# Kernel tuning notes

Hardware: AMD Instinct MI355X
Metric: run time of the kernel (lower is better)

Reference implementation:

```python
import jax, jax.numpy as jnp
import numpy as np

B, S, D = 4, 2048, 1024
H, E = 16, 64  # n_heads, head_size; H*E == D


def setup_inputs() -> dict:
    key = jax.random.key(0)
    ks = jax.random.split(key, 6)
    sd = 1.0 / np.sqrt(D)
    x = jax.random.normal(ks[0], (B, S, D), dtype=jnp.float32)
    # per-head Q/K/V projection weights, stacked: [H, D, E]
    Wq = jax.random.uniform(ks[1], (H, D, E), jnp.float32, -sd, sd)
    Wk = jax.random.uniform(ks[2], (H, D, E), jnp.float32, -sd, sd)
    Wv = jax.random.uniform(ks[3], (H, D, E), jnp.float32, -sd, sd)
    Wp = jax.random.uniform(ks[4], (D, D), jnp.float32, -sd, sd)
    bp = jax.random.uniform(ks[5], (D,), jnp.float32, -sd, sd)
    return {"x": x, "Wq": Wq, "Wk": Wk, "Wv": Wv, "Wp": Wp, "bp": bp}


def reference(x, Wq, Wk, Wv, Wp, bp):
    # Per-head projections (all heads batched): [B, H, S, E]
    q = jnp.einsum('bsd,hde->bhse', x, Wq)
    k = jnp.einsum('bsd,hde->bhse', x, Wk)
    v = jnp.einsum('bsd,hde->bhse', x, Wv)
    scale = E ** -0.5
    # Full causal score matrix [B, H, S, S]
    wei = jnp.einsum('bhse,bhte->bhst', q, k) * scale
    causal = jnp.tril(jnp.ones((S, S), dtype=bool))
    wei = jnp.where(causal, wei, -jnp.inf)
    wei = jax.nn.softmax(wei, axis=-1)
    out = jnp.einsum('bhst,bhte->bhse', wei, v)
    # concat heads along feature dim: [B, S, H*E]
    out = out.transpose(0, 2, 1, 3).reshape(B, S, H * E)
    # output projection (dropout is identity in eval)
    return out @ Wp.T + bp
```

## Files before the change

kernel.cpp:

```cpp
#include <hip/hip_runtime.h>

#define B_ 4
#define S_ 2048
#define D_ 1024
#define H_ 16
#define E_ 64
#define M_ (B_*S_)

typedef __attribute__((ext_vector_type(8))) short short8;
typedef __attribute__((ext_vector_type(4))) float floatx4;

#define GLD16(g, l) __builtin_amdgcn_global_load_lds( \
    (const __attribute__((address_space(1))) unsigned*)(g), \
    (__attribute__((address_space(3))) unsigned*)(l), 16, 0, 0)

__device__ __forceinline__ ushort f2b(float f) {
    union { float f; unsigned u; } v; v.f = f;
    unsigned r = v.u + 0x7fffu + ((v.u >> 16) & 1u);
    return (ushort)(r >> 16);
}
__device__ __forceinline__ unsigned cvt_pk_bf16(float lo, float hi) {
    unsigned r;
    asm("v_cvt_pk_bf16_f32 %0, %1, %2" : "=v"(r) : "v"(lo), "v"(hi));
    return r;
}
__device__ __forceinline__ float fast_exp2(float x) {
#if __has_builtin(__builtin_amdgcn_exp2f)
    return __builtin_amdgcn_exp2f(x);
#else
    float r; asm("v_exp_f32 %0, %1" : "=v"(r) : "v"(x)); return r;
#endif
}
__device__ __forceinline__ float lane_pull(float v, int srclane) {
    return __int_as_float(__builtin_amdgcn_ds_bpermute(srclane << 2, __float_as_int(v)));
}

__global__ __launch_bounds__(256) void cast_bf16(const float* __restrict__ in,
                                                 ushort* __restrict__ out, int n8) {
    int i = blockIdx.x * 256 + threadIdx.x;
    int stride = gridDim.x * 256;
    for (; i < n8; i += stride) {
        float4 a = ((const float4*)in)[2 * i];
        float4 b = ((const float4*)in)[2 * i + 1];
        short8 o;
        o[0] = (short)f2b(a.x); o[1] = (short)f2b(a.y);
        o[2] = (short)f2b(a.z); o[3] = (short)f2b(a.w);
        o[4] = (short)f2b(b.x); o[5] = (short)f2b(b.y);
        o[6] = (short)f2b(b.z); o[7] = (short)f2b(b.w);
        ((short8*)out)[i] = o;
    }
}

__global__ __launch_bounds__(256) void transpose_w(const float* __restrict__ Wq,
                                                   const float* __restrict__ Wk,
                                                   const float* __restrict__ Wv,
                                                   ushort* __restrict__ wt) {
    int g = blockIdx.y;
    int d0 = blockIdx.x * 64;
    const float* W = (g < 16 ? Wq : (g < 32 ? Wk : Wv)) + (size_t)(g & 15) * (D_ * E_);
    __shared__ __align__(16) ushort T[64 * 80];
    int t = threadIdx.x;
    #pragma unroll
    for (int it = 0; it < 4; ++it) {
        int i = it * 256 + t;
        int r = i >> 4, c = i & 15;
        float4 x = *(const float4*)(W + (size_t)(d0 + r) * E_ + c * 4);
        T[(c * 4 + 0) * 80 + r] = f2b(x.x);
        T[(c * 4 + 1) * 80 + r] = f2b(x.y);
        T[(c * 4 + 2) * 80 + r] = f2b(x.z);
        T[(c * 4 + 3) * 80 + r] = f2b(x.w);
    }
    __syncthreads();
    #pragma unroll
    for (int it = 0; it < 2; ++it) {
        int i = it * 256 + t;
        int e = i >> 3, c = i & 7;
        short8 x = *(const short8*)&T[e * 80 + c * 8];
        *(short8*)&wt[((size_t)g * E_ + e) * D_ + d0 + c * 8] = x;
    }
}

__global__ __launch_bounds__(512) void gemm_qkv(const ushort* __restrict__ xb,
                                                const ushort* __restrict__ wt,
                                                ushort* __restrict__ qk,
                                                ushort* __restrict__ vt) {
    const int m0 = blockIdx.x * 256;
    const int n0 = blockIdx.y * 128;
    const int w  = n0 >> 10;

    __shared__ __align__(16) ushort As[256 * 32];
    __shared__ __align__(16) ushort Bs[128 * 32];

    const int t = threadIdx.x, l = t & 63, wid = t >> 6;
    const int wm = (wid & 3) * 64, wn = (wid >> 2) * 64;
    floatx4 acc[4][4] = {};

    for (int k0 = 0; k0 < D_; k0 += 32) {
        __syncthreads();
        #pragma unroll
        for (int it = 0; it < 2; ++it) {
            int i = it * 512 + t;
            int r = i >> 2, cs = i & 3;
            int c = cs ^ ((r >> 1) & 3);
            GLD16(xb + (size_t)(m0 + r) * D_ + k0 + c * 8, &As[i * 8]);
        }
        {
            int r = t >> 2, cs = t & 3;
            int c = cs ^ ((r >> 1) & 3);
            GLD16(wt + (size_t)(n0 + r) * D_ + k0 + c * 8, &Bs[t * 8]);
        }
        __syncthreads();

        short8 af[4], bf[4];
        #pragma unroll
        for (int mf = 0; mf < 4; ++mf) {
            int row = wm + 16 * mf + (l & 15);
            int c = (l >> 4) ^ ((row >> 1) & 3);
            af[mf] = *(const short8*)&As[row * 32 + c * 8];
        }
        #pragma unroll
        for (int nf = 0; nf < 4; ++nf) {
            int row = wn + 16 * nf + (l & 15);
            int c = (l >> 4) ^ ((row >> 1) & 3);
            bf[nf] = *(const short8*)&Bs[row * 32 + c * 8];
        }
        #pragma unroll
        for (int mf = 0; mf < 4; ++mf)
            #pragma unroll
            for (int nf = 0; nf < 4; ++nf)
                acc[mf][nf] = __builtin_amdgcn_mfma_f32_16x16x32_bf16(af[mf], bf[nf], acc[mf][nf], 0, 0, 0);
    }

    if (w < 2) {
        ushort* outw = qk + (size_t)w * ((size_t)B_ * H_ * S_ * E_);
        #pragma unroll
        for (int mf = 0; mf < 4; ++mf)
            #pragma unroll
            for (int nf = 0; nf < 4; ++nf) {
                int n = n0 + wn + 16 * nf + (l & 15);
                int h = (n >> 6) & 15, e = n & 63;
                #pragma unroll
                for (int r = 0; r < 4; ++r) {
                    int m = m0 + wm + 16 * mf + (l >> 4) * 4 + r;
                    int b = m >> 11, s = m & (S_ - 1);
                    outw[((size_t)((b << 4) + h) * S_ + s) * E_ + e] = f2b(acc[mf][nf][r]);
                }
            }
    } else {
        #pragma unroll
        for (int mf = 0; mf < 4; ++mf) {
            int m = m0 + wm + 16 * mf + (l >> 4) * 4;
            int b = m >> 11, s = m & (S_ - 1);
            #pragma unroll
            for (int nf = 0; nf < 4; ++nf) {
                int n = n0 + wn + 16 * nf + (l & 15);
                int h = (n >> 6) & 15, e = n & 63;
                unsigned pk0 = cvt_pk_bf16(acc[mf][nf][0], acc[mf][nf][1]);
                unsigned pk1 = cvt_pk_bf16(acc[mf][nf][2], acc[mf][nf][3]);
                *(uint2*)&vt[((size_t)((b << 4) + h) * E_ + e) * S_ + s] = make_uint2(pk0, pk1);
            }
        }
    }
}

__global__ __launch_bounds__(256) void flash(const ushort* __restrict__ qg,
                                             const ushort* __restrict__ kg,
                                             const ushort* __restrict__ vtg,
                                             ushort* __restrict__ attn) {
    const int n = blockIdx.x;
    const int x = n >> 6;
    const int bh = n & 63;
    const int b = bh >> 4, h = bh & 15;
    const ushort* qb = qg + (size_t)bh * (S_ * E_);
    const ushort* kb = kg + (size_t)bh * (S_ * E_);
    const ushort* vb = vtg + (size_t)bh * (E_ * S_);

    __shared__ __align__(16) ushort QP[64 * 64];
    __shared__ __align__(16) ushort Ks[2][64 * 64];
    __shared__ __align__(16) ushort Vs[2][64 * 64];

    const int t = threadIdx.x, l = t & 63, wid = t >> 6;
    const float SC = 0.18033688f;
    const float NEG_INF = -__builtin_inff();
    const int g = l >> 4;
    const int qloc = l & 15;
    const int qts[2] = {x, 31 - x};
    ushort* Pw = &QP[wid * 1024];

    #pragma unroll 1
    for (int qi = 0; qi < 2; ++qi) {
        const int qt = qts[qi];

        #pragma unroll
        for (int it = 0; it < 2; ++it) {
            int i = it * 256 + t;
            int r = i >> 3, cs = i & 7, c = cs ^ (r & 7);
            GLD16(qb + (size_t)(qt * 64 + r) * E_ + c * 8, &QP[i * 8]);
            GLD16(kb + (size_t)r * E_ + c * 8, &Ks[0][i * 8]);
            GLD16(vb + (size_t)r * S_ + c * 8, &Vs[0][i * 8]);
        }
        __syncthreads();

        short8 qf[2];
        #pragma unroll
        for (int ks = 0; ks < 2; ++ks) {
            int row = wid * 16 + qloc;
            int c = (g + 4 * ks) ^ (row & 7);
            qf[ks] = *(const short8*)&QP[row * 64 + c * 8];
        }

        floatx4 o[4] = {};
        float mr = NEG_INF, lr = 0.f;

        int buf = 0;
        for (int jt = 0; jt <= qt; ++jt) {
            if (jt < qt) {
                #pragma unroll
                for (int it = 0; it < 2; ++it) {
                    int i = it * 256 + t;
                    int r = i >> 3, cs = i & 7, c = cs ^ (r & 7);
                    GLD16(kb + (size_t)((jt + 1) * 64 + r) * E_ + c * 8, &Ks[buf ^ 1][i * 8]);
                    GLD16(vb + (size_t)r * S_ + (jt + 1) * 64 + c * 8, &Vs[buf ^ 1][i * 8]);
                }
            }

            floatx4 s[4] = {};
            #pragma unroll
            for (int nf = 0; nf < 4; ++nf) {
                #pragma unroll
                for (int ks = 0; ks < 2; ++ks) {
                    int row = 16 * nf + qloc;
                    int c = (g + 4 * ks) ^ (row & 7);
                    short8 kf = *(const short8*)&Ks[buf][row * 64 + c * 8];
                    s[nf] = __builtin_amdgcn_mfma_f32_16x16x32_bf16(kf, qf[ks], s[nf], 0, 0, 0);
                }
            }

            if (jt == qt) {
                int qrow = wid * 16 + qloc;
                #pragma unroll
                for (int nf = 0; nf < 4; ++nf)
                    #pragma unroll
                    for (int r = 0; r < 4; ++r)
                        if (16 * nf + 4 * g + r > qrow) s[nf][r] = NEG_INF;
            }

            float mx = s[0][0];
            #pragma unroll
            for (int nf = 0; nf < 4; ++nf)
                #pragma unroll
                for (int r = 0; r < 4; ++r) mx = fmaxf(mx, s[nf][r]);
            mx = fmaxf(mx, __shfl_xor(mx, 16));
            mx = fmaxf(mx, __shfl_xor(mx, 32));
            bool ok = (mx - mr) * SC <= 8.0f;

            if (!__all(ok)) {
                float mn = fmaxf(mr, mx);
                float al = fast_exp2((mr - mn) * SC);
                mr = mn;
                lr *= al;
                #pragma unroll
                for (int r = 0; r < 4; ++r) {
                    float alq = lane_pull(al, 4 * g + r);
                    #pragma unroll
                    for (int nf = 0; nf < 4; ++nf) o[nf][r] *= alq;
                }
            }

            {
                float nm = -mr * SC;
                float rs = 0.f;
                #pragma unroll
                for (int nf = 0; nf < 4; ++nf)
                    #pragma unroll
                    for (int r = 0; r < 4; ++r) {
                        float p = fast_exp2(fmaf(s[nf][r], SC, nm));
                        s[nf][r] = p;
                        rs += p;
                    }
                lr += rs;
            }

            #pragma unroll
            for (int nf = 0; nf < 4; ++nf) {
                unsigned pk0 = cvt_pk_bf16(s[nf][0], s[nf][1]);
                unsigned pk1 = cvt_pk_bf16(s[nf][2], s[nf][3]);
                int chunk = 2 * nf + (g >> 1);
                int sw = chunk ^ (qloc & 7);
                int a = qloc * 64 + sw * 8 + 4 * (g & 1);
                *(uint2*)&Pw[a] = make_uint2(pk0, pk1);
            }

            short8 pf[2];
            #pragma unroll
            for (int ks = 0; ks < 2; ++ks) {
                int row = l & 15;
                int c = (g + 4 * ks) ^ (row & 7);
                pf[ks] = *(const short8*)&Pw[row * 64 + c * 8];
            }
            #pragma unroll
            for (int nf = 0; nf < 4; ++nf) {
                #pragma unroll
                for (int ks = 0; ks < 2; ++ks) {
                    int row = 16 * nf + (l & 15);
                    int c = (g + 4 * ks) ^ (row & 7);
                    short8 vf = *(const short8*)&Vs[buf][row * 64 + c * 8];
                    o[nf] = __builtin_amdgcn_mfma_f32_16x16x32_bf16(pf[ks], vf, o[nf], 0, 0, 0);
                }
            }

            __syncthreads();
            buf ^= 1;
        }

        lr += __shfl_xor(lr, 16);
        lr += __shfl_xor(lr, 32);
        float inv = 1.0f / lr;
        float il[4];
        #pragma unroll
        for (int r = 0; r < 4; ++r) il[r] = lane_pull(inv, 4 * g + r);

        #pragma unroll
        for (int nf = 0; nf < 4; ++nf) {
            int col = 16 * nf + qloc;
            #pragma unroll
            for (int rp = 0; rp < 2; ++rp) {
                unsigned pk = cvt_pk_bf16(o[nf][2 * rp] * il[2 * rp],
                                          o[nf][2 * rp + 1] * il[2 * rp + 1]);
                int row0 = g * 4 + 2 * rp;
                int a0 = row0 * 64 + (((col >> 3)) ^ (row0 & 7)) * 8 + (col & 7);
                int a1 = (row0 + 1) * 64 + (((col >> 3)) ^ ((row0 + 1) & 7)) * 8 + (col & 7);
                Pw[a0] = (ushort)pk;
                Pw[a1] = (ushort)(pk >> 16);
            }
        }
        #pragma unroll
        for (int it = 0; it < 2; ++it) {
            int i = it * 64 + l;
            int row = i >> 3, cc = i & 7;
            int c = cc ^ (row & 7);
            short8 vv = *(const short8*)&Pw[row * 64 + c * 8];
            int s_abs = qt * 64 + wid * 16 + row;
            *(short8*)&attn[((size_t)(b * S_ + s_abs)) * D_ + h * E_ + cc * 8] = vv;
        }
        __syncthreads();
    }
}

__global__ __launch_bounds__(256) void out_proj(const ushort* __restrict__ a,
                                                const ushort* __restrict__ wpb,
                                                const float* __restrict__ bp,
                                                float* __restrict__ out) {
    const int m0 = blockIdx.x * 128;
    const int n0 = blockIdx.y * 128;

    __shared__ __align__(16) ushort As[128 * 32];
    __shared__ __align__(16) ushort Bs[128 * 32];

    const int t = threadIdx.x, l = t & 63, wid = t >> 6;
    const int wm = (wid & 1) * 64, wn = (wid >> 1) * 64;
    floatx4 acc[4][4] = {};

    for (int k0 = 0; k0 < D_; k0 += 32) {
        __syncthreads();
        #pragma unroll
        for (int it = 0; it < 2; ++it) {
            int i = it * 256 + t;
            int r = i >> 2, cs = i & 3;
            int c = cs ^ ((r >> 1) & 3);
            GLD16(a + (size_t)(m0 + r) * D_ + k0 + c * 8, &As[i * 8]);
            GLD16(wpb + (size_t)(n0 + r) * D_ + k0 + c * 8, &Bs[i * 8]);
        }
        __syncthreads();

        short8 af[4], bf[4];
        #pragma unroll
        for (int mf = 0; mf < 4; ++mf) {
            int row = wm + 16 * mf + (l & 15);
            int c = (l >> 4) ^ ((row >> 1) & 3);
            af[mf] = *(const short8*)&As[row * 32 + c * 8];
        }
        #pragma unroll
        for (int nf = 0; nf < 4; ++nf) {
            int row = wn + 16 * nf + (l & 15);
            int c = (l >> 4) ^ ((row >> 1) & 3);
            bf[nf] = *(const short8*)&Bs[row * 32 + c * 8];
        }
        #pragma unroll
        for (int mf = 0; mf < 4; ++mf)
            #pragma unroll
            for (int nf = 0; nf < 4; ++nf)
                acc[mf][nf] = __builtin_amdgcn_mfma_f32_16x16x32_bf16(af[mf], bf[nf], acc[mf][nf], 0, 0, 0);
    }

    #pragma unroll
    for (int nf = 0; nf < 4; ++nf) {
        int col = n0 + wn + 16 * nf + (l & 15);
        float bias = bp[col];
        #pragma unroll
        for (int mf = 0; mf < 4; ++mf)
            #pragma unroll
            for (int r = 0; r < 4; ++r) {
                int m = m0 + wm + 16 * mf + (l >> 4) * 4 + r;
                out[(size_t)m * D_ + col] = acc[mf][nf][r] + bias;
            }
    }
}

extern "C" void kernel_launch(void* const* d_in, const int* in_sizes, int n_in,
                              void* d_out, int out_size, void* d_ws, size_t ws_size,
                              hipStream_t stream) {
    const float* x  = (const float*)d_in[0];
    const float* Wq = (const float*)d_in[1];
    const float* Wk = (const float*)d_in[2];
    const float* Wv = (const float*)d_in[3];
    const float* Wp = (const float*)d_in[4];
    const float* bp = (const float*)d_in[5];

    ushort* ws = (ushort*)d_ws;
    const size_t NX  = (size_t)M_ * D_;
    const size_t NW  = (size_t)48 * E_ * D_;
    const size_t NP  = (size_t)D_ * D_;
    const size_t QSZ = (size_t)B_ * H_ * S_ * E_;
    ushort* xb    = ws;
    ushort* wt    = xb + NX;
    ushort* wpb   = wt + NW;
    ushort* qk    = wpb + NP;
    ushort* vt    = qk + 2 * QSZ;
    ushort* attnb = vt + QSZ;

    cast_bf16  <<<2048, 256, 0, stream>>>(x, xb, (int)(NX / 8));
    cast_bf16  <<<512, 256, 0, stream>>>(Wp, wpb, (int)(NP / 8));
    transpose_w<<<dim3(16, 48), 256, 0, stream>>>(Wq, Wk, Wv, wt);
    gemm_qkv   <<<dim3(M_ / 256, 24), 512, 0, stream>>>(xb, wt, qk, vt);
    flash      <<<1024, 256, 0, stream>>>(qk, qk + QSZ, vt, attnb);
    out_proj   <<<dim3(M_ / 128, D_ / 128), 256, 0, stream>>>(attnb, wpb, bp, (float*)d_out);
}
```

Before: 185.1 us.

## Enlarge flash-attention query tile to 128 rows with two sub-tiles per wave

Each flash block now processes a 128-row query super-tile instead of 64 rows. Each wave carries two 16-row query fragments, each with its own running max, sum and output accumulators. Every K/V tile loaded into shared memory is therefore reused across twice as many query rows, which halves global K/V traffic and barrier count per query row. The grid is halved to 512 blocks and causal load balancing still pairs super-tiles x and 15-x. In exchange, register and LDS use per block rise and there are fewer blocks to fill the CUs, which could reduce occupancy and latency hiding.

```diff
diff --git a/kernel.cpp b/kernel.cpp
--- a/kernel.cpp
+++ b/kernel.cpp
@@ -175,7 +175,7 @@
     const ushort* kb = kg + (size_t)bh * (S_ * E_);
     const ushort* vb = vtg + (size_t)bh * (E_ * S_);
 
-    __shared__ __align__(16) ushort QP[64 * 64];
+    __shared__ __align__(16) ushort QP[128 * 64];
     __shared__ __align__(16) ushort Ks[2][64 * 64];
     __shared__ __align__(16) ushort Vs[2][64 * 64];
 
@@ -184,37 +184,47 @@
     const float NEG_INF = -__builtin_inff();
     const int g = l >> 4;
     const int qloc = l & 15;
-    const int qts[2] = {x, 31 - x};
-    ushort* Pw = &QP[wid * 1024];
+    const int sups[2] = {x, 15 - x};
+    ushort* Pw = &QP[wid * 2048];
 
     #pragma unroll 1
     for (int qi = 0; qi < 2; ++qi) {
-        const int qt = qts[qi];
-
+        const int sup = sups[qi];
+        const int ntiles = 2 * sup + 2;
+
+        #pragma unroll
+        for (int it = 0; it < 4; ++it) {
+            int i = it * 256 + t;
+            int r = i >> 3, cs = i & 7, c = cs ^ (r & 7);
+            GLD16(qb + (size_t)(sup * 128 + r) * E_ + c * 8, &QP[i * 8]);
+        }
         #pragma unroll
         for (int it = 0; it < 2; ++it) {
             int i = it * 256 + t;
             int r = i >> 3, cs = i & 7, c = cs ^ (r & 7);
-            GLD16(qb + (size_t)(qt * 64 + r) * E_ + c * 8, &QP[i * 8]);
             GLD16(kb + (size_t)r * E_ + c * 8, &Ks[0][i * 8]);
             GLD16(vb + (size_t)r * S_ + c * 8, &Vs[0][i * 8]);
         }
         __syncthreads();
 
-        short8 qf[2];
-        #pragma unroll
-        for (int ks = 0; ks < 2; ++ks) {
-            int row = wid * 16 + qloc;
-            int c = (g + 4 * ks) ^ (row & 7);
-            qf[ks] = *(const short8*)&QP[row * 64 + c * 8];
-        }
-
-        floatx4 o[4] = {};
-        float mr = NEG_INF, lr = 0.f;
+        short8 qf[2][2];
+        #pragma unroll
+        for (int m = 0; m < 2; ++m)
+            #pragma unroll
+            for (int ks = 0; ks < 2; ++ks) {
+                int row = wid * 32 + m * 16 + qloc;
+                int c = (g + 4 * ks) ^ (row & 7);
+                qf[m][ks] = *(const short8*)&QP[row * 64 + c * 8];
+            }
+
+        floatx4 o[2][4] = {};
+        float mr[2], lr[2];
+        #pragma unroll
+        for (int m = 0; m < 2; ++m) { mr[m] = NEG_INF; lr[m] = 0.f; }
 
         int buf = 0;
-        for (int jt = 0; jt <= qt; ++jt) {
-            if (jt < qt) {
+        for (int jt = 0; jt < ntiles; ++jt) {
+            if (jt + 1 < ntiles) {
                 #pragma unroll
                 for (int it = 0; it < 2; ++it) {
                     int i = it * 256 + t;
@@ -224,7 +234,7 @@
                 }
             }
 
-            floatx4 s[4] = {};
+            floatx4 s[2][4] = {};
             #pragma unroll
             for (int nf = 0; nf < 4; ++nf) {
                 #pragma unroll
@@ -232,72 +242,90 @@
                     int row = 16 * nf + qloc;
                     int c = (g + 4 * ks) ^ (row & 7);
                     short8 kf = *(const short8*)&Ks[buf][row * 64 + c * 8];
-                    s[nf] = __builtin_amdgcn_mfma_f32_16x16x32_bf16(kf, qf[ks], s[nf], 0, 0, 0);
-                }
-            }
-
-            if (jt == qt) {
-                int qrow = wid * 16 + qloc;
+                    s[0][nf] = __builtin_amdgcn_mfma_f32_16x16x32_bf16(kf, qf[0][ks], s[0][nf], 0, 0, 0);
+                    s[1][nf] = __builtin_amdgcn_mfma_f32_16x16x32_bf16(kf, qf[1][ks], s[1][nf], 0, 0, 0);
+                }
+            }
+
+            if (jt >= 2 * sup) {
+                int kvbase = jt * 64;
+                #pragma unroll
+                for (int m = 0; m < 2; ++m) {
+                    int qrow = sup * 128 + wid * 32 + m * 16 + qloc;
+                    #pragma unroll
+                    for (int nf = 0; nf < 4; ++nf)
+                        #pragma unroll
+                        for (int r = 0; r < 4; ++r)
+                            if (kvbase + 16 * nf + 4 * g + r > qrow) s[m][nf][r] = NEG_INF;
+                }
+            }
+
+            float mxm[2]; bool ok = true;
+            #pragma unroll
+            for (int m = 0; m < 2; ++m) {
+                float mx = s[m][0][0];
                 #pragma unroll
                 for (int nf = 0; nf < 4; ++nf)
                     #pragma unroll
-                    for (int r = 0; r < 4; ++r)
-                        if (16 * nf + 4 * g + r > qrow) s[nf][r] = NEG_INF;
-            }
-
-            float mx = s[0][0];
-            #pragma unroll
-            for (int nf = 0; nf < 4; ++nf)
-                #pragma unroll
-                for (int r = 0; r < 4; ++r) mx = fmaxf(mx, s[nf][r]);
-            mx = fmaxf(mx, __shfl_xor(mx, 16));
-            mx = fmaxf(mx, __shfl_xor(mx, 32));
-            bool ok = (mx - mr) * SC <= 8.0f;
+                    for (int r = 0; r < 4; ++r) mx = fmaxf(mx, s[m][nf][r]);
+                mx = fmaxf(mx, __shfl_xor(mx, 16));
+                mx = fmaxf(mx, __shfl_xor(mx, 32));
+                mxm[m] = mx;
+                ok = ok && ((mx - mr[m]) * SC <= 8.0f);
+            }
 
             if (!__all(ok)) {
-                float mn = fmaxf(mr, mx);
-                float al = fast_exp2((mr - mn) * SC);
-                mr = mn;
-                lr *= al;
-                #pragma unroll
-                for (int r = 0; r < 4; ++r) {
-                    float alq = lane_pull(al, 4 * g + r);
+                #pragma unroll
+                for (int m = 0; m < 2; ++m) {
+                    float mn = fmaxf(mr[m], mxm[m]);
+                    float al = fast_exp2((mr[m] - mn) * SC);
+                    mr[m] = mn;
+                    lr[m] *= al;
                     #pragma unroll
-                    for (int nf = 0; nf < 4; ++nf) o[nf][r] *= alq;
-                }
-            }
-
-            {
-                float nm = -mr * SC;
+                    for (int r = 0; r < 4; ++r) {
+                        float alq = lane_pull(al, 4 * g + r);
+                        #pragma unroll
+                        for (int nf = 0; nf < 4; ++nf) o[m][nf][r] *= alq;
+                    }
+                }
+            }
+
+            #pragma unroll
+            for (int m = 0; m < 2; ++m) {
+                float nm = -mr[m] * SC;
                 float rs = 0.f;
                 #pragma unroll
                 for (int nf = 0; nf < 4; ++nf)
                     #pragma unroll
                     for (int r = 0; r < 4; ++r) {
-                        float p = fast_exp2(fmaf(s[nf][r], SC, nm));
-                        s[nf][r] = p;
+                        float p = fast_exp2(fmaf(s[m][nf][r], SC, nm));
+                        s[m][nf][r] = p;
                         rs += p;
                     }
-                lr += rs;
-            }
-
-            #pragma unroll
-            for (int nf = 0; nf < 4; ++nf) {
-                unsigned pk0 = cvt_pk_bf16(s[nf][0], s[nf][1]);
-                unsigned pk1 = cvt_pk_bf16(s[nf][2], s[nf][3]);
-                int chunk = 2 * nf + (g >> 1);
-                int sw = chunk ^ (qloc & 7);
-                int a = qloc * 64 + sw * 8 + 4 * (g & 1);
-                *(uint2*)&Pw[a] = make_uint2(pk0, pk1);
-            }
-
-            short8 pf[2];
-            #pragma unroll
-            for (int ks = 0; ks < 2; ++ks) {
-                int row = l & 15;
-                int c = (g + 4 * ks) ^ (row & 7);
-                pf[ks] = *(const short8*)&Pw[row * 64 + c * 8];
-            }
+                lr[m] += rs;
+            }
+
+            #pragma unroll
+            for (int m = 0; m < 2; ++m)
+                #pragma unroll
+                for (int nf = 0; nf < 4; ++nf) {
+                    unsigned pk0 = cvt_pk_bf16(s[m][nf][0], s[m][nf][1]);
+                    unsigned pk1 = cvt_pk_bf16(s[m][nf][2], s[m][nf][3]);
+                    int chunk = 2 * nf + (g >> 1);
+                    int sw = chunk ^ (qloc & 7);
+                    int a = qloc * 64 + sw * 8 + 4 * (g & 1);
+                    *(uint2*)&Pw[m * 1024 + a] = make_uint2(pk0, pk1);
+                }
+
+            short8 pf[2][2];
+            #pragma unroll
+            for (int m = 0; m < 2; ++m)
+                #pragma unroll
+                for (int ks = 0; ks < 2; ++ks) {
+                    int row = l & 15;
+                    int c = (g + 4 * ks) ^ (row & 7);
+                    pf[m][ks] = *(const short8*)&Pw[m * 1024 + row * 64 + c * 8];
+                }
             #pragma unroll
             for (int nf = 0; nf < 4; ++nf) {
                 #pragma unroll
@@ -305,7 +333,8 @@
                     int row = 16 * nf + (l & 15);
                     int c = (g + 4 * ks) ^ (row & 7);
                     short8 vf = *(const short8*)&Vs[buf][row * 64 + c * 8];
-                    o[nf] = __builtin_amdgcn_mfma_f32_16x16x32_bf16(pf[ks], vf, o[nf], 0, 0, 0);
+                    o[0][nf] = __builtin_amdgcn_mfma_f32_16x16x32_bf16(pf[0][ks], vf, o[0][nf], 0, 0, 0);
+                    o[1][nf] = __builtin_amdgcn_mfma_f32_16x16x32_bf16(pf[1][ks], vf, o[1][nf], 0, 0, 0);
                 }
             }
 
@@ -313,34 +342,39 @@
             buf ^= 1;
         }
 
-        lr += __shfl_xor(lr, 16);
-        lr += __shfl_xor(lr, 32);
-        float inv = 1.0f / lr;
-        float il[4];
-        #pragma unroll
-        for (int r = 0; r < 4; ++r) il[r] = lane_pull(inv, 4 * g + r);
-
-        #pragma unroll
-        for (int nf = 0; nf < 4; ++nf) {
-            int col = 16 * nf + qloc;
-            #pragma unroll
-            for (int rp = 0; rp < 2; ++rp) {
-                unsigned pk = cvt_pk_bf16(o[nf][2 * rp] * il[2 * rp],
-                                          o[nf][2 * rp + 1] * il[2 * rp + 1]);
-                int row0 = g * 4 + 2 * rp;
-                int a0 = row0 * 64 + (((col >> 3)) ^ (row0 & 7)) * 8 + (col & 7);
-                int a1 = (row0 + 1) * 64 + (((col >> 3)) ^ ((row0 + 1) & 7)) * 8 + (col & 7);
-                Pw[a0] = (ushort)pk;
-                Pw[a1] = (ushort)(pk >> 16);
-            }
-        }
-        #pragma unroll
-        for (int it = 0; it < 2; ++it) {
+        float il[2][4];
+        #pragma unroll
+        for (int m = 0; m < 2; ++m) {
+            lr[m] += __shfl_xor(lr[m], 16);
+            lr[m] += __shfl_xor(lr[m], 32);
+            float inv = 1.0f / lr[m];
+            #pragma unroll
+            for (int r = 0; r < 4; ++r) il[m][r] = lane_pull(inv, 4 * g + r);
+        }
+
+        #pragma unroll
+        for (int m = 0; m < 2; ++m)
+            #pragma unroll
+            for (int nf = 0; nf < 4; ++nf) {
+                int col = 16 * nf + qloc;
+                #pragma unroll
+                for (int rp = 0; rp < 2; ++rp) {
+                    unsigned pk = cvt_pk_bf16(o[m][nf][2 * rp] * il[m][2 * rp],
+                                              o[m][nf][2 * rp + 1] * il[m][2 * rp + 1]);
+                    int row0 = g * 4 + 2 * rp;
+                    int a0 = row0 * 64 + (((col >> 3)) ^ (row0 & 7)) * 8 + (col & 7);
+                    int a1 = (row0 + 1) * 64 + (((col >> 3)) ^ ((row0 + 1) & 7)) * 8 + (col & 7);
+                    Pw[m * 1024 + a0] = (ushort)pk;
+                    Pw[m * 1024 + a1] = (ushort)(pk >> 16);
+                }
+            }
+        #pragma unroll
+        for (int it = 0; it < 4; ++it) {
             int i = it * 64 + l;
             int row = i >> 3, cc = i & 7;
             int c = cc ^ (row & 7);
             short8 vv = *(const short8*)&Pw[row * 64 + c * 8];
-            int s_abs = qt * 64 + wid * 16 + row;
+            int s_abs = sup * 128 + wid * 32 + row;
             *(short8*)&attn[((size_t)(b * S_ + s_abs)) * D_ + h * E_ + cc * 8] = vv;
         }
         __syncthreads();
@@ -433,6 +467,6 @@
     cast_bf16  <<<512, 256, 0, stream>>>(Wp, wpb, (int)(NP / 8));
     transpose_w<<<dim3(16, 48), 256, 0, stream>>>(Wq, Wk, Wv, wt);
     gemm_qkv   <<<dim3(M_ / 256, 24), 512, 0, stream>>>(xb, wt, qk, vt);
-    flash      <<<1024, 256, 0, stream>>>(qk, qk + QSZ, vt, attnb);
+    flash      <<<512, 256, 0, stream>>>(qk, qk + QSZ, vt, attnb);
     out_proj   <<<dim3(M_ / 128, D_ / 128), 256, 0, stream>>>(attnb, wpb, bp, (float*)d_out);
 }
```

Result: slower. 207.6 us (+12.1%).
